# Kernel tuning notes

Measured on AMD Instinct MI355X. Metric: run time of the kernel, lower is better.

## Reference

```python
import jax, jax.numpy as jnp
import numpy as np

N_NODES = 100000
N_GRAPHS = 64


def _gcn_norm(edge_index, num_nodes):
    # Add self-loops and compute symmetric normalization (PyG GCNConv gcn_norm).
    src = jnp.concatenate([edge_index[0], jnp.arange(num_nodes, dtype=edge_index.dtype)])
    dst = jnp.concatenate([edge_index[1], jnp.arange(num_nodes, dtype=edge_index.dtype)])
    deg = jax.ops.segment_sum(jnp.ones_like(dst, dtype=jnp.float32), dst, num_segments=num_nodes)
    dinv = jnp.where(deg > 0, jax.lax.rsqrt(deg), 0.0)
    norm = dinv[src] * dinv[dst]  # [E + N]
    return src, dst, norm


def _gcn_conv(x, src, dst, norm, W, b, num_nodes):
    h = x @ W                                   # [N, out]
    msg = h[src] * norm[:, None]                # gather + scale  [E+N, out]
    out = jax.ops.segment_sum(msg, dst, num_segments=num_nodes)  # scatter-add
    return out + b


def setup_inputs() -> dict:
    key = jax.random.key(0)
    ks = jax.random.split(key, 8)
    E = 1600000
    pos = jax.random.normal(ks[0], (N_NODES, 3), dtype=jnp.float32)
    edge_index = jax.random.randint(ks[1], (2, E), 0, N_NODES, dtype=jnp.int64)
    batch = jnp.sort(jax.random.randint(ks[2], (N_NODES,), 0, N_GRAPHS, dtype=jnp.int64))
    def glorot(k, shape):
        lim = np.sqrt(6.0 / (shape[0] + shape[1])).astype(np.float32)
        return jax.random.uniform(k, shape, dtype=jnp.float32, minval=-lim, maxval=lim)
    return {
        "pos": pos,
        "edge_index": edge_index,
        "batch": batch,
        "W1": glorot(ks[3], (3, 64)),  "b1": jnp.zeros((64,), jnp.float32),
        "W2": glorot(ks[4], (64, 64)), "b2": jnp.zeros((64,), jnp.float32),
        "W3": glorot(ks[5], (64, 24)), "b3": jnp.zeros((24,), jnp.float32),
    }


def reference(pos, edge_index, batch, W1, b1, W2, b2, W3, b3):
    src, dst, norm = _gcn_norm(edge_index, N_NODES)
    h = jax.nn.relu(_gcn_conv(pos, src, dst, norm, W1, b1, N_NODES))
    h = jax.nn.relu(_gcn_conv(h, src, dst, norm, W2, b2, N_NODES))
    y = _gcn_conv(h, src, dst, norm, W3, b3, N_NODES)  # [N, 24]
    # global_mean_pool over batch ids, then tanh
    sums = jax.ops.segment_sum(y, batch, num_segments=N_GRAPHS)          # [G, 24]
    counts = jax.ops.segment_sum(jnp.ones((N_NODES,), jnp.float32), batch, num_segments=N_GRAPHS)
    mean = sums / jnp.maximum(counts, 1.0)[:, None]
    return jnp.tanh(mean)
```

## Files before the change

### kernel.cpp

```cpp
#include <hip/hip_runtime.h>
#include <math.h>

#define NNODES 100000
#define NGRAPHS 64
#define NB 391
#define CAP 4608
#define NBLK3 1216


__device__ __forceinline__ unsigned int f2bf(float x) {
    union { float f; unsigned int u; } v;
    v.f = x;
    unsigned int r = v.u + 0x7FFFu + ((v.u >> 16) & 1u);
    return r >> 16;
}
__device__ __forceinline__ unsigned int pack2bf(float lo, float hi) {
    return f2bf(lo) | (f2bf(hi) << 16);
}
__device__ __forceinline__ float bflo(unsigned int u) {
    union { unsigned int u; float f; } v;
    v.u = u << 16;
    return v.f;
}
__device__ __forceinline__ float bfhi(unsigned int u) {
    union { unsigned int u; float f; } v;
    v.u = u & 0xFFFF0000u;
    return v.f;
}


__global__ void bucket_scatter(const int* __restrict__ src, const int* __restrict__ dst,
                               int* __restrict__ bCur, unsigned int* __restrict__ packed,
                               int E) {
    __shared__ int h[NB];
    __shared__ int cur[NB];
    for (int k = threadIdx.x; k < NB; k += 256) h[k] = 0;
    __syncthreads();
    int base = blockIdx.x * 2048 + threadIdx.x;
    int d[8], s[8], b[8];
#pragma unroll
    for (int k = 0; k < 8; ++k) {
        int e = base + k * 256;
        if (e < E) {
            d[k] = dst[e];
            s[k] = src[e];
            b[k] = d[k] >> 8;
            atomicAdd(&h[b[k]], 1);
        }
    }
    __syncthreads();
    for (int k = threadIdx.x; k < NB; k += 256) {
        int c = h[k];
        cur[k] = c ? atomicAdd(&bCur[k], c) : 0;
    }
    __syncthreads();
#pragma unroll
    for (int k = 0; k < 8; ++k) {
        int e = base + k * 256;
        if (e < E) {
            int pos = atomicAdd(&cur[b[k]], 1);
            if (pos < CAP)
                packed[(size_t)b[k] * CAP + pos] = ((unsigned int)(d[k] & 255) << 17) | (unsigned int)s[k];
        }
    }
}

__global__ void bucket_build(const unsigned int* __restrict__ packed, const int* __restrict__ bCur,
                             const int* __restrict__ batch, const float* __restrict__ pos,
                             int2* __restrict__ rowBE, int* __restrict__ col,
                             float* __restrict__ dinv, int2* __restrict__ dg,
                             float4* __restrict__ pos4, int N_) {
    __shared__ int cnt[256];
    __shared__ int bas[256];
    int tid = threadIdx.x;
    int b = blockIdx.x;
    int count = bCur[b];
    if (count > CAP) count = CAP;
    int beg = b * CAP;
    cnt[tid] = 0;
    __syncthreads();
    for (int k = beg + tid; k < beg + count; k += 256) atomicAdd(&cnt[packed[k] >> 17], 1);
    __syncthreads();
    int myCnt = cnt[tid];
    bas[tid] = myCnt;
    __syncthreads();
    for (int off = 1; off < 256; off <<= 1) {
        int v = (tid >= off) ? bas[tid - off] : 0;
        __syncthreads();
        bas[tid] += v;
        __syncthreads();
    }
    int excl = beg + ((tid > 0) ? bas[tid - 1] : 0);
    int node = (b << 8) + tid;
    if (node < N_) {
        rowBE[node] = make_int2(excl, excl + myCnt);
        float di = rsqrtf((float)myCnt + 1.0f);
        dinv[node] = di;
        dg[node] = make_int2(__float_as_int(di), batch[node]);
        pos4[node] = make_float4(pos[node * 3] * di, pos[node * 3 + 1] * di,
                                 pos[node * 3 + 2] * di, di);
    }
    __syncthreads();
    bas[tid] = excl;
    __syncthreads();
    for (int k = beg + tid; k < beg + count; k += 256) {
        unsigned int p = packed[k];
        int pos_ = atomicAdd(&bas[p >> 17], 1);
        col[pos_] = (int)(p & 0x1FFFFu);
    }
}


__global__ void mm12_gp(const float4* __restrict__ pos4, const int2* __restrict__ rowBE,
                        const int* __restrict__ col, const float* __restrict__ dinv,
                        const float* __restrict__ W1, const float* __restrict__ b1,
                        const float* __restrict__ W2, uint2* __restrict__ outb, int n) {
    __shared__ float4 part[256];
    __shared__ float4 ag[64];
    __shared__ float xs[64][65];
    __shared__ float4 ws[64 * 16];
    const int tid = threadIdx.x;
    const int rowBase = blockIdx.x * 64;
    const int r = tid >> 2, t4 = tid & 3;
    const int i = rowBase + r;

    float sx = 0, sy = 0, sz = 0, dival = 0;
    if (i < n) {
        int2 be = rowBE[i];
        float4 ps = pos4[i];
        dival = ps.w;
        if (t4 == 0) { sx = ps.x; sy = ps.y; sz = ps.z; }
        for (int j = be.x + t4; j < be.y; j += 4) {
            float4 v = pos4[col[j]];
            sx += v.x; sy += v.y; sz += v.z;
        }
    }
    part[tid] = make_float4(sx, sy, sz, dival);
    const float4* W24 = (const float4*)W2;
    for (int idx = tid; idx < 64 * 16; idx += 256) ws[idx] = W24[idx];
    __syncthreads();
    if (tid < 64) {
        float4 p0 = part[tid * 4], p1 = part[tid * 4 + 1];
        float4 p2 = part[tid * 4 + 2], p3 = part[tid * 4 + 3];
        ag[tid] = make_float4((p0.x + p1.x) + (p2.x + p3.x),
                              (p0.y + p1.y) + (p2.y + p3.y),
                              (p0.z + p1.z) + (p2.z + p3.z), p0.w);
    }
    __syncthreads();
    for (int idx = tid; idx < 64 * 64; idx += 256) {
        int rr = idx >> 6;
        int k = idx & 63;
        float4 a = ag[rr];
        float v = b1[k] + a.w * (a.x * W1[k] + a.y * W1[64 + k] + a.z * W1[128 + k]);
        xs[rr][k] = fmaxf(v, 0.0f);
    }
    __syncthreads();

    const int f4 = tid & 15;
    const int r0 = (tid >> 4) * 4;
    float4 a0 = make_float4(0, 0, 0, 0), a1 = a0, a2 = a0, a3 = a0;
#pragma unroll 4
    for (int k = 0; k < 64; ++k) {
        float4 wv = ws[k * 16 + f4];
        float xa = xs[r0 + 0][k];
        float xb = xs[r0 + 1][k];
        float xc = xs[r0 + 2][k];
        float xd = xs[r0 + 3][k];
        a0.x += wv.x * xa; a0.y += wv.y * xa; a0.z += wv.z * xa; a0.w += wv.w * xa;
        a1.x += wv.x * xb; a1.y += wv.y * xb; a1.z += wv.z * xb; a1.w += wv.w * xb;
        a2.x += wv.x * xc; a2.y += wv.y * xc; a2.z += wv.z * xc; a2.w += wv.w * xc;
        a3.x += wv.x * xd; a3.y += wv.y * xd; a3.z += wv.z * xd; a3.w += wv.w * xd;
    }
    int i0 = rowBase + r0;
    float d0 = (i0 + 0 < n) ? dinv[i0 + 0] : 1.0f;
    float d1 = (i0 + 1 < n) ? dinv[i0 + 1] : 1.0f;
    float d2 = (i0 + 2 < n) ? dinv[i0 + 2] : 1.0f;
    float d3 = (i0 + 3 < n) ? dinv[i0 + 3] : 1.0f;
    if (i0 + 0 < n)
        outb[(size_t)(i0 + 0) * 16 + f4] = make_uint2(pack2bf(a0.x * d0, a0.y * d0), pack2bf(a0.z * d0, a0.w * d0));
    if (i0 + 1 < n)
        outb[(size_t)(i0 + 1) * 16 + f4] = make_uint2(pack2bf(a1.x * d1, a1.y * d1), pack2bf(a1.z * d1, a1.w * d1));
    if (i0 + 2 < n)
        outb[(size_t)(i0 + 2) * 16 + f4] = make_uint2(pack2bf(a2.x * d2, a2.y * d2), pack2bf(a2.z * d2, a2.w * d2));
    if (i0 + 3 < n)
        outb[(size_t)(i0 + 3) * 16 + f4] = make_uint2(pack2bf(a3.x * d3, a3.y * d3), pack2bf(a3.z * d3, a3.w * d3));
}


__global__ void gather2_b16(const int2* __restrict__ rowBE, const int* __restrict__ col,
                            const uint4* __restrict__ h, const float* __restrict__ dinv,
                            const float* __restrict__ bias, uint4* __restrict__ outb, int n) {
    int t = blockIdx.x * blockDim.x + threadIdx.x;
    if (t >= n * 8) return;
    int i = t >> 3;
    int c8 = t & 7;
    float di = dinv[i];
    int2 be = rowBE[i];
    float acc[8];
    {
        uint4 sv = h[t];
        acc[0] = bflo(sv.x); acc[1] = bfhi(sv.x);
        acc[2] = bflo(sv.y); acc[3] = bfhi(sv.y);
        acc[4] = bflo(sv.z); acc[5] = bfhi(sv.z);
        acc[6] = bflo(sv.w); acc[7] = bfhi(sv.w);
    }
    int j = be.x;
    for (; j + 8 <= be.y; j += 8) {
        int s[8];
        uint4 v[8];
#pragma unroll
        for (int k = 0; k < 8; ++k) s[k] = col[j + k];
#pragma unroll
        for (int k = 0; k < 8; ++k) v[k] = h[(size_t)s[k] * 8 + c8];
#pragma unroll
        for (int k = 0; k < 8; ++k) {
            acc[0] += bflo(v[k].x); acc[1] += bfhi(v[k].x);
            acc[2] += bflo(v[k].y); acc[3] += bfhi(v[k].y);
            acc[4] += bflo(v[k].z); acc[5] += bfhi(v[k].z);
            acc[6] += bflo(v[k].w); acc[7] += bfhi(v[k].w);
        }
    }
    for (; j < be.y; ++j) {
        uint4 v = h[(size_t)col[j] * 8 + c8];
        acc[0] += bflo(v.x); acc[1] += bfhi(v.x);
        acc[2] += bflo(v.y); acc[3] += bfhi(v.y);
        acc[4] += bflo(v.z); acc[5] += bfhi(v.z);
        acc[6] += bflo(v.w); acc[7] += bfhi(v.w);
    }
    const float* bv = bias + c8 * 8;
#pragma unroll
    for (int k = 0; k < 8; ++k) acc[k] = fmaxf(acc[k] * di + bv[k], 0.0f);
    outb[t] = make_uint4(pack2bf(acc[0], acc[1]), pack2bf(acc[2], acc[3]),
                         pack2bf(acc[4], acc[5]), pack2bf(acc[6], acc[7]));
}


__global__ void mm3_b16(const uint4* __restrict__ xb, const float* __restrict__ W,
                        const float* __restrict__ dinv, uint2* __restrict__ outb, int n) {
    __shared__ float xs[128][65];
    __shared__ float4 ws[64 * 6];
    const int tid = threadIdx.x;
    const int rowBase = blockIdx.x * 128;

    for (int idx = tid; idx < 128 * 8; idx += 192) {
        int r = idx >> 3;
        int c8 = idx & 7;
        int gr = rowBase + r;
        uint4 v = (gr < n) ? xb[(size_t)gr * 8 + c8] : make_uint4(0, 0, 0, 0);
        float* xp = &xs[r][c8 * 8];
        xp[0] = bflo(v.x); xp[1] = bfhi(v.x);
        xp[2] = bflo(v.y); xp[3] = bfhi(v.y);
        xp[4] = bflo(v.z); xp[5] = bfhi(v.z);
        xp[6] = bflo(v.w); xp[7] = bfhi(v.w);
    }
    const float4* W4 = (const float4*)W;
    for (int idx = tid; idx < 64 * 6; idx += 192) ws[idx] = W4[idx];
    __syncthreads();

    const int f4 = tid % 6;
    const int r0 = (tid / 6) * 4;
    float4 a0 = make_float4(0, 0, 0, 0), a1 = a0, a2 = a0, a3 = a0;
#pragma unroll 4
    for (int k = 0; k < 64; ++k) {
        float4 wv = ws[k * 6 + f4];
        float xa = xs[r0 + 0][k];
        float xb_ = xs[r0 + 1][k];
        float xc = xs[r0 + 2][k];
        float xd = xs[r0 + 3][k];
        a0.x += wv.x * xa; a0.y += wv.y * xa; a0.z += wv.z * xa; a0.w += wv.w * xa;
        a1.x += wv.x * xb_; a1.y += wv.y * xb_; a1.z += wv.z * xb_; a1.w += wv.w * xb_;
        a2.x += wv.x * xc; a2.y += wv.y * xc; a2.z += wv.z * xc; a2.w += wv.w * xc;
        a3.x += wv.x * xd; a3.y += wv.y * xd; a3.z += wv.z * xd; a3.w += wv.w * xd;
    }
    int i0 = rowBase + r0;
    float d0 = (i0 + 0 < n) ? dinv[i0 + 0] : 1.0f;
    float d1 = (i0 + 1 < n) ? dinv[i0 + 1] : 1.0f;
    float d2 = (i0 + 2 < n) ? dinv[i0 + 2] : 1.0f;
    float d3 = (i0 + 3 < n) ? dinv[i0 + 3] : 1.0f;
    if (i0 + 0 < n)
        outb[(size_t)(i0 + 0) * 6 + f4] = make_uint2(pack2bf(a0.x * d0, a0.y * d0), pack2bf(a0.z * d0, a0.w * d0));
    if (i0 + 1 < n)
        outb[(size_t)(i0 + 1) * 6 + f4] = make_uint2(pack2bf(a1.x * d1, a1.y * d1), pack2bf(a1.z * d1, a1.w * d1));
    if (i0 + 2 < n)
        outb[(size_t)(i0 + 2) * 6 + f4] = make_uint2(pack2bf(a2.x * d2, a2.y * d2), pack2bf(a2.z * d2, a2.w * d2));
    if (i0 + 3 < n)
        outb[(size_t)(i0 + 3) * 6 + f4] = make_uint2(pack2bf(a3.x * d3, a3.y * d3), pack2bf(a3.z * d3, a3.w * d3));
}


__global__ void gather3_pool(const int2* __restrict__ rowBE, const int* __restrict__ col,
                             const uint4* __restrict__ y0, const int2* __restrict__ dg,
                             float* __restrict__ partials, float* __restrict__ cpart, int n) {
    __shared__ float lpool[NGRAPHS * 24];
    __shared__ float lcnt[NGRAPHS];
    for (int k = threadIdx.x; k < NGRAPHS * 24; k += 256) lpool[k] = 0.0f;
    for (int k = threadIdx.x; k < NGRAPHS; k += 256) lcnt[k] = 0.0f;
    __syncthreads();

    const int T = n * 6;
    const int stride = NBLK3 * 256;
    for (int t = blockIdx.x * 256 + threadIdx.x; t < T; t += stride) {
        int i = t / 6;
        int q = t - i * 6;
        int r = q >> 1;
        int half = q & 1;
        int2 wi = dg[i];
        float di = __int_as_float(wi.x);
        int g = wi.y;
        int2 be = rowBE[i];
        int mid = be.x + ((be.y - be.x + 1) >> 1);
        int a = half ? mid : be.x;
        int b = half ? be.y : mid;
        float acc[8] = {0, 0, 0, 0, 0, 0, 0, 0};
        if (!half) {
            uint4 sv = y0[(size_t)i * 3 + r];
            acc[0] = bflo(sv.x); acc[1] = bfhi(sv.x);
            acc[2] = bflo(sv.y); acc[3] = bfhi(sv.y);
            acc[4] = bflo(sv.z); acc[5] = bfhi(sv.z);
            acc[6] = bflo(sv.w); acc[7] = bfhi(sv.w);
        }
        int j = a;
        for (; j + 8 <= b; j += 8) {
            int s[8];
            uint4 v[8];
#pragma unroll
            for (int k = 0; k < 8; ++k) s[k] = col[j + k];
#pragma unroll
            for (int k = 0; k < 8; ++k) v[k] = y0[(size_t)s[k] * 3 + r];
#pragma unroll
            for (int k = 0; k < 8; ++k) {
                acc[0] += bflo(v[k].x); acc[1] += bfhi(v[k].x);
                acc[2] += bflo(v[k].y); acc[3] += bfhi(v[k].y);
                acc[4] += bflo(v[k].z); acc[5] += bfhi(v[k].z);
                acc[6] += bflo(v[k].w); acc[7] += bfhi(v[k].w);
            }
        }
        for (; j < b; ++j) {
            uint4 v = y0[(size_t)col[j] * 3 + r];
            acc[0] += bflo(v.x); acc[1] += bfhi(v.x);
            acc[2] += bflo(v.y); acc[3] += bfhi(v.y);
            acc[4] += bflo(v.z); acc[5] += bfhi(v.z);
            acc[6] += bflo(v.w); acc[7] += bfhi(v.w);
        }
        float* lp = &lpool[g * 24 + r * 8];
#pragma unroll
        for (int k = 0; k < 8; ++k) atomicAdd(&lp[k], acc[k] * di);
        if (q == 0) atomicAdd(&lcnt[g], 1.0f);
    }
    __syncthreads();
    float* pp = partials + (size_t)blockIdx.x * (NGRAPHS * 24);
    for (int k = threadIdx.x; k < NGRAPHS * 24; k += 256) pp[k] = lpool[k];
    float* cp = cpart + (size_t)blockIdx.x * NGRAPHS;
    for (int k = threadIdx.x; k < NGRAPHS; k += 256) cp[k] = lcnt[k];
}

__global__ void pool_finish(const float* __restrict__ partials, const float* __restrict__ cpart,
                            const float* __restrict__ b3, float* __restrict__ out) {
    int w = blockIdx.x * 4 + (threadIdx.x >> 6);
    int lane = threadIdx.x & 63;
    if (w >= NGRAPHS * 24) return;
    int g = w / 24;
    int c = w - g * 24;
    float s = 0.0f, cn = 0.0f;
    for (int b = lane; b < NBLK3; b += 64) {
        s += partials[(size_t)b * (NGRAPHS * 24) + w];
        cn += cpart[(size_t)b * NGRAPHS + g];
    }
#pragma unroll
    for (int off = 32; off > 0; off >>= 1) {
        s += __shfl_down(s, off);
        cn += __shfl_down(cn, off);
    }
    if (lane == 0) out[w] = tanhf(s / fmaxf(cn, 1.0f) + b3[c]);
}


static inline int gridFor(long long total, int block) {
    return (int)((total + block - 1) / block);
}

extern "C" void kernel_launch(void* const* d_in, const int* in_sizes, int n_in,
                              void* d_out, int out_size, void* d_ws, size_t ws_size,
                              hipStream_t stream) {
    const float* pos   = (const float*)d_in[0];
    const int*   ei    = (const int*)d_in[1];
    const int*   batch = (const int*)d_in[2];
    const float* W1    = (const float*)d_in[3];
    const float* b1    = (const float*)d_in[4];
    const float* W2    = (const float*)d_in[5];
    const float* b2    = (const float*)d_in[6];
    const float* W3    = (const float*)d_in[7];
    const float* b3    = (const float*)d_in[8];
    float*       out   = (float*)d_out;

    const int N = NNODES;
    const int E = in_sizes[1] / 2;
    const int* src = ei;
    const int* dst = ei + E;

    char* p = (char*)d_ws;
    uint4*  z2b    = (uint4*)p;         p += (size_t)N * 8 * sizeof(uint4);
    uint4*  h2b    = (uint4*)p;         p += (size_t)N * 8 * sizeof(uint4);
    uint4*  y0b    = (uint4*)p;         p += (size_t)N * 3 * sizeof(uint4);
    float4* pos4   = (float4*)p;        p += (size_t)N * sizeof(float4);
    float*  partials = (float*)p;       p += (size_t)NBLK3 * NGRAPHS * 24 * sizeof(float);
    float*  cpart  = (float*)p;         p += (size_t)NBLK3 * NGRAPHS * sizeof(float);
    int2*   rowBE  = (int2*)p;          p += (size_t)N * sizeof(int2);
    int2*   dg     = (int2*)p;          p += (size_t)N * sizeof(int2);
    float*  dinv   = (float*)p;         p += (size_t)N * sizeof(float);
    int*    bCur   = (int*)p;           p += NB * sizeof(int);
    unsigned int* packed = (unsigned int*)p;  p += (size_t)NB * CAP * sizeof(unsigned int);
    int*    col    = (int*)p;           p += (size_t)NB * CAP * sizeof(int);

    const int B = 256;
    const int edgeBlocks = gridFor(E, 2048);

    hipMemsetAsync(bCur, 0, NB * sizeof(int), stream);
    bucket_scatter<<<edgeBlocks, 256, 0, stream>>>(src, dst, bCur, packed, E);
    bucket_build<<<NB, 256, 0, stream>>>(packed, bCur, batch, pos, rowBE, col, dinv, dg, pos4, N);

    mm12_gp<<<gridFor(N, 64), 256, 0, stream>>>(pos4, rowBE, col, dinv, W1, b1, W2, (uint2*)z2b, N);

    gather2_b16<<<gridFor((long long)N * 8, B), B, 0, stream>>>(rowBE, col, z2b, dinv, b2, h2b, N);

    mm3_b16<<<gridFor(N, 128), 192, 0, stream>>>(h2b, W3, dinv, (uint2*)y0b, N);
    gather3_pool<<<NBLK3, 256, 0, stream>>>(rowBE, col, y0b, dg, partials, cpart, N);
    pool_finish<<<gridFor((long long)NGRAPHS * 24 * 64, B), B, 0, stream>>>(partials, cpart, b3, out);
}
```

Before: 264.6 us.

## Split layer-3 features into 16+8 column planes with separate gather-pool kernels

The 24-column layer-3 output is now stored as two arrays, a 16-wide plane and an 8-wide plane, so each gather pass reads power-of-two strides. Each plane is aggregated by its own kernel. Edge halves are combined with a lane shuffle before a single shared-memory atomic, which halves the atomics. Index and row-bound loads now use nontemporal loads to reduce cache pollution, and the pool partials reuse the z2b workspace. The cost is an extra kernel launch and a second pass over the CSR indices.

After: 265.3 us. No clear change (+0.3%).

```diff
diff --git a/kernel.cpp b/kernel.cpp
--- a/kernel.cpp
+++ b/kernel.cpp
@@ -5,7 +5,8 @@
 #define NGRAPHS 64
 #define NB 391
 #define CAP 4608
-#define NBLK3 1216
+#define NBLKA 1024
+#define NBLKB 512
 
 
 __device__ __forceinline__ unsigned int f2bf(float x) {
@@ -26,6 +27,16 @@
     union { unsigned int u; float f; } v;
     v.u = u & 0xFFFF0000u;
     return v.f;
+}
+
+
+__device__ __forceinline__ int ntld(const int* p) { return __builtin_nontemporal_load(p); }
+__device__ __forceinline__ int2 ntld2(const int2* p) {
+    long long v = __builtin_nontemporal_load((const long long*)p);
+    int2 r;
+    r.x = (int)(unsigned int)(v & 0xffffffffLL);
+    r.y = (int)(v >> 32);
+    return r;
 }
 
 
@@ -131,7 +142,7 @@
         dival = ps.w;
         if (t4 == 0) { sx = ps.x; sy = ps.y; sz = ps.z; }
         for (int j = be.x + t4; j < be.y; j += 4) {
-            float4 v = pos4[col[j]];
+            float4 v = pos4[ntld(&col[j])];
             sx += v.x; sy += v.y; sz += v.z;
         }
     }
@@ -209,7 +220,7 @@
         int s[8];
         uint4 v[8];
 #pragma unroll
-        for (int k = 0; k < 8; ++k) s[k] = col[j + k];
+        for (int k = 0; k < 8; ++k) s[k] = ntld(&col[j + k]);
 #pragma unroll
         for (int k = 0; k < 8; ++k) v[k] = h[(size_t)s[k] * 8 + c8];
 #pragma unroll
@@ -221,7 +232,7 @@
         }
     }
     for (; j < be.y; ++j) {
-        uint4 v = h[(size_t)col[j] * 8 + c8];
+        uint4 v = h[(size_t)ntld(&col[j]) * 8 + c8];
         acc[0] += bflo(v.x); acc[1] += bfhi(v.x);
         acc[2] += bflo(v.y); acc[3] += bfhi(v.y);
         acc[4] += bflo(v.z); acc[5] += bfhi(v.z);
@@ -235,8 +246,15 @@
 }
 
 
+__device__ __forceinline__ void st_y(uint2* __restrict__ yA, uint2* __restrict__ yB,
+                                     int i, int f4, uint2 v) {
+    if (f4 < 4) yA[(size_t)i * 4 + f4] = v;
+    else        yB[(size_t)i * 2 + (f4 - 4)] = v;
+}
+
 __global__ void mm3_b16(const uint4* __restrict__ xb, const float* __restrict__ W,
-                        const float* __restrict__ dinv, uint2* __restrict__ outb, int n) {
+                        const float* __restrict__ dinv, uint2* __restrict__ yA,
+                        uint2* __restrict__ yB, int n) {
     __shared__ float xs[128][65];
     __shared__ float4 ws[64 * 6];
     const int tid = threadIdx.x;
@@ -278,42 +296,39 @@
     float d2 = (i0 + 2 < n) ? dinv[i0 + 2] : 1.0f;
     float d3 = (i0 + 3 < n) ? dinv[i0 + 3] : 1.0f;
     if (i0 + 0 < n)
-        outb[(size_t)(i0 + 0) * 6 + f4] = make_uint2(pack2bf(a0.x * d0, a0.y * d0), pack2bf(a0.z * d0, a0.w * d0));
+        st_y(yA, yB, i0 + 0, f4, make_uint2(pack2bf(a0.x * d0, a0.y * d0), pack2bf(a0.z * d0, a0.w * d0)));
     if (i0 + 1 < n)
-        outb[(size_t)(i0 + 1) * 6 + f4] = make_uint2(pack2bf(a1.x * d1, a1.y * d1), pack2bf(a1.z * d1, a1.w * d1));
+        st_y(yA, yB, i0 + 1, f4, make_uint2(pack2bf(a1.x * d1, a1.y * d1), pack2bf(a1.z * d1, a1.w * d1)));
     if (i0 + 2 < n)
-        outb[(size_t)(i0 + 2) * 6 + f4] = make_uint2(pack2bf(a2.x * d2, a2.y * d2), pack2bf(a2.z * d2, a2.w * d2));
+        st_y(yA, yB, i0 + 2, f4, make_uint2(pack2bf(a2.x * d2, a2.y * d2), pack2bf(a2.z * d2, a2.w * d2)));
     if (i0 + 3 < n)
-        outb[(size_t)(i0 + 3) * 6 + f4] = make_uint2(pack2bf(a3.x * d3, a3.y * d3), pack2bf(a3.z * d3, a3.w * d3));
-}
-
-
-__global__ void gather3_pool(const int2* __restrict__ rowBE, const int* __restrict__ col,
-                             const uint4* __restrict__ y0, const int2* __restrict__ dg,
-                             float* __restrict__ partials, float* __restrict__ cpart, int n) {
-    __shared__ float lpool[NGRAPHS * 24];
-    __shared__ float lcnt[NGRAPHS];
-    for (int k = threadIdx.x; k < NGRAPHS * 24; k += 256) lpool[k] = 0.0f;
-    for (int k = threadIdx.x; k < NGRAPHS; k += 256) lcnt[k] = 0.0f;
-    __syncthreads();
-
-    const int T = n * 6;
-    const int stride = NBLK3 * 256;
+        st_y(yA, yB, i0 + 3, f4, make_uint2(pack2bf(a3.x * d3, a3.y * d3), pack2bf(a3.z * d3, a3.w * d3)));
+}
+
+
+__global__ void gather3A(const int2* __restrict__ rowBE, const int* __restrict__ col,
+                         const uint4* __restrict__ yA, const int2* __restrict__ dg,
+                         float* __restrict__ partA) {
+    __shared__ float lpool[NGRAPHS * 16];
+    for (int k = threadIdx.x; k < NGRAPHS * 16; k += 256) lpool[k] = 0.0f;
+    __syncthreads();
+
+    const int T = NNODES * 4;
+    const int stride = NBLKA * 256;
     for (int t = blockIdx.x * 256 + threadIdx.x; t < T; t += stride) {
-        int i = t / 6;
-        int q = t - i * 6;
-        int r = q >> 1;
-        int half = q & 1;
-        int2 wi = dg[i];
+        int i = t >> 2;
+        int half = t & 1;
+        int r = (t >> 1) & 1;
+        int2 wi = ntld2(&dg[i]);
         float di = __int_as_float(wi.x);
         int g = wi.y;
-        int2 be = rowBE[i];
+        int2 be = ntld2(&rowBE[i]);
         int mid = be.x + ((be.y - be.x + 1) >> 1);
         int a = half ? mid : be.x;
         int b = half ? be.y : mid;
         float acc[8] = {0, 0, 0, 0, 0, 0, 0, 0};
         if (!half) {
-            uint4 sv = y0[(size_t)i * 3 + r];
+            uint4 sv = yA[(size_t)i * 2 + r];
             acc[0] = bflo(sv.x); acc[1] = bfhi(sv.x);
             acc[2] = bflo(sv.y); acc[3] = bfhi(sv.y);
             acc[4] = bflo(sv.z); acc[5] = bfhi(sv.z);
@@ -324,9 +339,9 @@
             int s[8];
             uint4 v[8];
 #pragma unroll
-            for (int k = 0; k < 8; ++k) s[k] = col[j + k];
-#pragma unroll
-            for (int k = 0; k < 8; ++k) v[k] = y0[(size_t)s[k] * 3 + r];
+            for (int k = 0; k < 8; ++k) s[k] = ntld(&col[j + k]);
+#pragma unroll
+            for (int k = 0; k < 8; ++k) v[k] = yA[(size_t)s[k] * 2 + r];
 #pragma unroll
             for (int k = 0; k < 8; ++k) {
                 acc[0] += bflo(v[k].x); acc[1] += bfhi(v[k].x);
@@ -336,36 +351,108 @@
             }
         }
         for (; j < b; ++j) {
-            uint4 v = y0[(size_t)col[j] * 3 + r];
+            uint4 v = yA[(size_t)ntld(&col[j]) * 2 + r];
             acc[0] += bflo(v.x); acc[1] += bfhi(v.x);
             acc[2] += bflo(v.y); acc[3] += bfhi(v.y);
             acc[4] += bflo(v.z); acc[5] += bfhi(v.z);
             acc[6] += bflo(v.w); acc[7] += bfhi(v.w);
         }
-        float* lp = &lpool[g * 24 + r * 8];
-#pragma unroll
-        for (int k = 0; k < 8; ++k) atomicAdd(&lp[k], acc[k] * di);
-        if (q == 0) atomicAdd(&lcnt[g], 1.0f);
-    }
-    __syncthreads();
-    float* pp = partials + (size_t)blockIdx.x * (NGRAPHS * 24);
-    for (int k = threadIdx.x; k < NGRAPHS * 24; k += 256) pp[k] = lpool[k];
+#pragma unroll
+        for (int k = 0; k < 8; ++k) acc[k] += __shfl_xor(acc[k], 1);
+        if (!half) {
+            float* lp = &lpool[g * 16 + r * 8];
+#pragma unroll
+            for (int k = 0; k < 8; ++k) atomicAdd(&lp[k], acc[k] * di);
+        }
+    }
+    __syncthreads();
+    float* pp = partA + (size_t)blockIdx.x * (NGRAPHS * 16);
+    for (int k = threadIdx.x; k < NGRAPHS * 16; k += 256) pp[k] = lpool[k];
+}
+
+__global__ void gather3B(const int2* __restrict__ rowBE, const int* __restrict__ col,
+                         const uint4* __restrict__ yB, const int2* __restrict__ dg,
+                         float* __restrict__ partB, float* __restrict__ cpart) {
+    __shared__ float lpool[NGRAPHS * 8];
+    __shared__ float lcnt[NGRAPHS];
+    for (int k = threadIdx.x; k < NGRAPHS * 8; k += 256) lpool[k] = 0.0f;
+    for (int k = threadIdx.x; k < NGRAPHS; k += 256) lcnt[k] = 0.0f;
+    __syncthreads();
+
+    const int T = NNODES * 2;
+    const int stride = NBLKB * 256;
+    for (int t = blockIdx.x * 256 + threadIdx.x; t < T; t += stride) {
+        int i = t >> 1;
+        int half = t & 1;
+        int2 wi = ntld2(&dg[i]);
+        float di = __int_as_float(wi.x);
+        int g = wi.y;
+        int2 be = ntld2(&rowBE[i]);
+        int mid = be.x + ((be.y - be.x + 1) >> 1);
+        int a = half ? mid : be.x;
+        int b = half ? be.y : mid;
+        float acc[8] = {0, 0, 0, 0, 0, 0, 0, 0};
+        if (!half) {
+            uint4 sv = yB[i];
+            acc[0] = bflo(sv.x); acc[1] = bfhi(sv.x);
+            acc[2] = bflo(sv.y); acc[3] = bfhi(sv.y);
+            acc[4] = bflo(sv.z); acc[5] = bfhi(sv.z);
+            acc[6] = bflo(sv.w); acc[7] = bfhi(sv.w);
+        }
+        int j = a;
+        for (; j + 8 <= b; j += 8) {
+            int s[8];
+            uint4 v[8];
+#pragma unroll
+            for (int k = 0; k < 8; ++k) s[k] = ntld(&col[j + k]);
+#pragma unroll
+            for (int k = 0; k < 8; ++k) v[k] = yB[s[k]];
+#pragma unroll
+            for (int k = 0; k < 8; ++k) {
+                acc[0] += bflo(v[k].x); acc[1] += bfhi(v[k].x);
+                acc[2] += bflo(v[k].y); acc[3] += bfhi(v[k].y);
+                acc[4] += bflo(v[k].z); acc[5] += bfhi(v[k].z);
+                acc[6] += bflo(v[k].w); acc[7] += bfhi(v[k].w);
+            }
+        }
+        for (; j < b; ++j) {
+            uint4 v = yB[ntld(&col[j])];
+            acc[0] += bflo(v.x); acc[1] += bfhi(v.x);
+            acc[2] += bflo(v.y); acc[3] += bfhi(v.y);
+            acc[4] += bflo(v.z); acc[5] += bfhi(v.z);
+            acc[6] += bflo(v.w); acc[7] += bfhi(v.w);
+        }
+#pragma unroll
+        for (int k = 0; k < 8; ++k) acc[k] += __shfl_xor(acc[k], 1);
+        if (!half) {
+            float* lp = &lpool[g * 8];
+#pragma unroll
+            for (int k = 0; k < 8; ++k) atomicAdd(&lp[k], acc[k] * di);
+            atomicAdd(&lcnt[g], 1.0f);
+        }
+    }
+    __syncthreads();
+    float* pp = partB + (size_t)blockIdx.x * (NGRAPHS * 8);
+    for (int k = threadIdx.x; k < NGRAPHS * 8; k += 256) pp[k] = lpool[k];
     float* cp = cpart + (size_t)blockIdx.x * NGRAPHS;
     for (int k = threadIdx.x; k < NGRAPHS; k += 256) cp[k] = lcnt[k];
 }
 
-__global__ void pool_finish(const float* __restrict__ partials, const float* __restrict__ cpart,
-                            const float* __restrict__ b3, float* __restrict__ out) {
+__global__ void pool_finish(const float* __restrict__ partA, const float* __restrict__ partB,
+                            const float* __restrict__ cpart, const float* __restrict__ b3,
+                            float* __restrict__ out) {
     int w = blockIdx.x * 4 + (threadIdx.x >> 6);
     int lane = threadIdx.x & 63;
     if (w >= NGRAPHS * 24) return;
     int g = w / 24;
     int c = w - g * 24;
     float s = 0.0f, cn = 0.0f;
-    for (int b = lane; b < NBLK3; b += 64) {
-        s += partials[(size_t)b * (NGRAPHS * 24) + w];
-        cn += cpart[(size_t)b * NGRAPHS + g];
-    }
+    if (c < 16) {
+        for (int b = lane; b < NBLKA; b += 64) s += partA[(size_t)b * (NGRAPHS * 16) + g * 16 + c];
+    } else {
+        for (int b = lane; b < NBLKB; b += 64) s += partB[(size_t)b * (NGRAPHS * 8) + g * 8 + (c - 16)];
+    }
+    for (int b = lane; b < NBLKB; b += 64) cn += cpart[(size_t)b * NGRAPHS + g];
 #pragma unroll
     for (int off = 32; off > 0; off >>= 1) {
         s += __shfl_down(s, off);
@@ -401,16 +488,18 @@
     char* p = (char*)d_ws;
     uint4*  z2b    = (uint4*)p;         p += (size_t)N * 8 * sizeof(uint4);
     uint4*  h2b    = (uint4*)p;         p += (size_t)N * 8 * sizeof(uint4);
-    uint4*  y0b    = (uint4*)p;         p += (size_t)N * 3 * sizeof(uint4);
+    uint4*  yA     = (uint4*)p;         p += (size_t)N * 2 * sizeof(uint4);
+    uint4*  yB     = (uint4*)p;         p += (size_t)N * 1 * sizeof(uint4);
     float4* pos4   = (float4*)p;        p += (size_t)N * sizeof(float4);
-    float*  partials = (float*)p;       p += (size_t)NBLK3 * NGRAPHS * 24 * sizeof(float);
-    float*  cpart  = (float*)p;         p += (size_t)NBLK3 * NGRAPHS * sizeof(float);
     int2*   rowBE  = (int2*)p;          p += (size_t)N * sizeof(int2);
     int2*   dg     = (int2*)p;          p += (size_t)N * sizeof(int2);
     float*  dinv   = (float*)p;         p += (size_t)N * sizeof(float);
     int*    bCur   = (int*)p;           p += NB * sizeof(int);
     unsigned int* packed = (unsigned int*)p;  p += (size_t)NB * CAP * sizeof(unsigned int);
     int*    col    = (int*)p;           p += (size_t)NB * CAP * sizeof(int);
+    float*  partA  = (float*)z2b;
+    float*  partB  = partA + (size_t)NBLKA * NGRAPHS * 16;
+    float*  cpartB = partB + (size_t)NBLKB * NGRAPHS * 8;
 
     const int B = 256;
     const int edgeBlocks = gridFor(E, 2048);
@@ -423,7 +512,8 @@
 
     gather2_b16<<<gridFor((long long)N * 8, B), B, 0, stream>>>(rowBE, col, z2b, dinv, b2, h2b, N);
 
-    mm3_b16<<<gridFor(N, 128), 192, 0, stream>>>(h2b, W3, dinv, (uint2*)y0b, N);
-    gather3_pool<<<NBLK3, 256, 0, stream>>>(rowBE, col, y0b, dg, partials, cpart, N);
-    pool_finish<<<gridFor((long long)NGRAPHS * 24 * 64, B), B, 0, stream>>>(partials, cpart, b3, out);
-}
+    mm3_b16<<<gridFor(N, 128), 192, 0, stream>>>(h2b, W3, dinv, (uint2*)yA, (uint2*)yB, N);
+    gather3A<<<NBLKA, 256, 0, stream>>>(rowBE, col, yA, dg, partA);
+    gather3B<<<NBLKB, 256, 0, stream>>>(rowBE, col, yB, dg, partB, cpartB);
+    pool_finish<<<gridFor((long long)NGRAPHS * 24 * 64, B), B, 0, stream>>>(partA, partB, cpartB, b3, out);
+}
```
